# Kernel tuning notes

Measured on AMD Instinct MI355X. Metric: run time of the kernel, lower is better.

Reference implementation:

```python
import jax, jax.numpy as jnp
import numpy as np

B, H, W, C = 8, 64, 64, 512
C8, C2 = C // 8, C // 2  # f/g channels = 64, h channels = 256 (divisor = 2)


def _maxpool2x2(t):
    # [B, H, W, F] -> [B, H//2, W//2, F], valid 2x2 max pooling
    b, h, w, f = t.shape
    return t.reshape(b, h // 2, 2, w // 2, 2, f).max(axis=(2, 4))


def setup_inputs() -> dict:
    key = jax.random.key(0)
    kx, kf, kg, kh, ko, kgam = jax.random.split(key, 6)
    sf = lambda fan_in: (1.0 / np.sqrt(fan_in)).astype(np.float32)
    return {
        "x": jax.random.normal(kx, (B, H, W, C), dtype=jnp.float32),
        "wf": jax.random.normal(kf, (C, C8), dtype=jnp.float32) * sf(C),
        "wg": jax.random.normal(kg, (C, C8), dtype=jnp.float32) * sf(C),
        "wh": jax.random.normal(kh, (C, C2), dtype=jnp.float32) * sf(C),
        "wo": jax.random.normal(ko, (C2, C), dtype=jnp.float32) * sf(C2),
        "gamma": jax.random.normal(kgam, (1,), dtype=jnp.float32) * 0.1,
    }


def reference(x, wf, wg, wh, wo, gamma):
    b = x.shape[0]
    # 1x1 convs == channel matmuls
    f = _maxpool2x2(jnp.einsum("bhwc,cd->bhwd", x, wf)).reshape(b, -1, C8)  # [B, N/4, C/8]
    g = jnp.einsum("bhwc,cd->bhwd", x, wg).reshape(b, -1, C8)               # [B, N,   C/8]
    s = jnp.einsum("bqd,bkd->bqk", g, f)                                     # unscaled scores
    beta = jax.nn.softmax(s, axis=-1)
    h = _maxpool2x2(jnp.einsum("bhwc,cd->bhwd", x, wh)).reshape(b, -1, C2)  # [B, N/4, C/2]
    o = jnp.einsum("bqk,bkd->bqd", beta, h).reshape(b, H, W, C2)
    o = jnp.einsum("bhwd,dc->bhwc", o, wo)                                   # o_conv back to C
    return gamma * o + x
```

## Files before the change

kernel.cpp:

```cpp
#include <hip/hip_runtime.h>
#include <hip/hip_bf16.h>

#define NTOK 4096
#define NPOOL 1024

using short8 = __attribute__((ext_vector_type(8))) short;
using f32x4  = __attribute__((ext_vector_type(4))) float;

__device__ __forceinline__ unsigned short f2bf(float f) {
  __hip_bfloat16 h = __float2bfloat16(f);
  return __builtin_bit_cast(unsigned short, h);
}

__device__ __forceinline__ int pool_row(int bx, int m) {
  int pg = bx * 16 + (m >> 2);
  int corner = m & 3;
  int batch = pg >> 10;
  int pl = pg & 1023;
  int pi = pl >> 5, pj = pl & 31;
  return (batch << 12) + ((2 * pi + (corner >> 1)) << 6) + 2 * pj + (corner & 1);
}

__global__ __launch_bounds__(256) void pack_w(const float* __restrict__ wf,
                                              const float* __restrict__ wg,
                                              const float* __restrict__ wh,
                                              const float* __restrict__ wo,
                                              unsigned short* __restrict__ wcatT,
                                              unsigned short* __restrict__ woT) {
  int i = blockIdx.x * 256 + threadIdx.x;
  if (i < 384 * 512) {
    int n = i >> 9, k = i & 511;
    float v = (n < 64) ? wf[k * 64 + n]
            : (n < 128) ? wg[k * 64 + (n - 64)]
                        : wh[k * 256 + (n - 128)];
    wcatT[i] = f2bf(v);
  } else if (i < 384 * 512 + 512 * 256) {
    int j = i - 384 * 512;
    int n = j >> 8, k = j & 255;
    woT[j] = f2bf(wo[(size_t)k * 512 + n]);
  }
}

__global__ __launch_bounds__(512) void fgh_proj(const float* __restrict__ x,
                                                const unsigned short* __restrict__ wcatT,
                                                unsigned short* __restrict__ fB,
                                                unsigned short* __restrict__ gB,
                                                unsigned short* __restrict__ hT) {
  __shared__ unsigned short lds[33280];
  const int tid = threadIdx.x;
  const int bx = blockIdx.x;
  const int wave = tid >> 6, lane = tid & 63;
  const int col = lane & 15, rgrp = lane >> 4;
  const int wcol = wave * 48;

  {
    const int xm = tid >> 3, xk4 = (tid & 7) << 2;
    const float* xrow = x + (size_t)pool_row(bx, xm) * 512 + xk4;
    unsigned short* dst = &lds[xm * 520 + xk4];
#pragma unroll
    for (int kt = 0; kt < 16; ++kt) {
      float4 v = *(const float4*)(xrow + kt * 32);
      ushort4 o4;
      o4.x = f2bf(v.x); o4.y = f2bf(v.y); o4.z = f2bf(v.z); o4.w = f2bf(v.w);
      *(ushort4*)(dst + kt * 32) = o4;
    }
  }
  __syncthreads();

  f32x4 acc[4][3];
#pragma unroll
  for (int mt = 0; mt < 4; ++mt)
#pragma unroll
    for (int nt = 0; nt < 3; ++nt) acc[mt][nt] = (f32x4){0.f, 0.f, 0.f, 0.f};

  for (int kt = 0; kt < 16; ++kt) {
    short8 am[4];
#pragma unroll
    for (int mt = 0; mt < 4; ++mt)
      am[mt] = *(const short8*)&lds[(mt * 16 + col) * 520 + kt * 32 + rgrp * 8];
#pragma unroll
    for (int nt = 0; nt < 3; ++nt) {
      short8 bn = *(const short8*)(wcatT + (size_t)(wcol + nt * 16 + col) * 512 + kt * 32 + rgrp * 8);
#pragma unroll
      for (int mt = 0; mt < 4; ++mt)
        acc[mt][nt] = __builtin_amdgcn_mfma_f32_16x16x32_bf16(am[mt], bn, acc[mt][nt], 0, 0, 0);
    }
  }
  __syncthreads();

  unsigned short* gO = lds;
  unsigned short* fO = lds + 4608;
  unsigned short* hO = lds + 5760;
#pragma unroll
  for (int mt = 0; mt < 4; ++mt) {
#pragma unroll
    for (int nt = 0; nt < 3; ++nt) {
      int n = wcol + nt * 16 + col;
      f32x4 a = acc[mt][nt];
      if (n < 64) {
        float mx = fmaxf(fmaxf(a[0], a[1]), fmaxf(a[2], a[3]));
        fO[(mt * 4 + rgrp) * 72 + n] = f2bf(mx);
      } else if (n < 128) {
#pragma unroll
        for (int reg = 0; reg < 4; ++reg)
          gO[(mt * 16 + rgrp * 4 + reg) * 72 + (n - 64)] = f2bf(a[reg]);
      } else {
        float mx = fmaxf(fmaxf(a[0], a[1]), fmaxf(a[2], a[3]));
        hO[(n - 128) * 24 + (mt * 4 + rgrp)] = f2bf(mx);
      }
    }
  }
  __syncthreads();

  const int b = bx >> 6, pkb = (bx & 63) * 16;
  {
    int m = tid >> 3, d8 = (tid & 7) << 3;
    *(uint4*)(gB + (size_t)pool_row(bx, m) * 64 + d8) = *(const uint4*)&gO[m * 72 + d8];
  }
  if (tid < 128) {
    int pr = tid >> 3, d8 = (tid & 7) << 3;
    *(uint4*)(fB + (size_t)(bx * 16 + pr) * 64 + d8) = *(const uint4*)&fO[pr * 72 + d8];
  }
  {
    int dv = tid >> 1, p8 = (tid & 1) << 3;
    *(uint4*)(hT + (((size_t)b * 256 + dv) << 10) + pkb + p8) = *(const uint4*)&hO[dv * 24 + p8];
  }
}

__global__ __launch_bounds__(512) void attn_mfma(const __hip_bfloat16* __restrict__ G,
                                                 const __hip_bfloat16* __restrict__ F,
                                                 const __hip_bfloat16* __restrict__ HT,
                                                 const unsigned short* __restrict__ woT,
                                                 const float* __restrict__ Xres,
                                                 const float* __restrict__ gamma,
                                                 float* __restrict__ Out) {
  __shared__ unsigned short lds[33792];

  const int tid = threadIdx.x;
  const int wave = tid >> 6, lane = tid & 63;
  const int col = lane & 15;
  const int rgrp = lane >> 4;
  const int b = blockIdx.x >> 5, qt = blockIdx.x & 31;

  const unsigned short* Gb = (const unsigned short*)G + ((size_t)b * NTOK + qt * 128) * 64;
  const unsigned short* Fb = (const unsigned short*)F + (size_t)b * NPOOL * 64;
  const unsigned short* Hb = (const unsigned short*)HT + (size_t)b * 256 * NPOOL;

  short8 ag[2];
#pragma unroll
  for (int ks = 0; ks < 2; ++ks)
    ag[ks] = *(const short8*)(Gb + (size_t)(wave * 16 + col) * 64 + ks * 32 + rgrp * 8);

  f32x4 oacc[16];
#pragma unroll
  for (int t = 0; t < 16; ++t) oacc[t] = (f32x4){0.f, 0.f, 0.f, 0.f};
  float m_run[4], l_run[4];
#pragma unroll
  for (int r = 0; r < 4; ++r) { m_run[r] = -1e30f; l_run[r] = 0.f; }

  const int fk = tid >> 3, fd8 = (tid & 7) << 3;

  for (int kc = 0; kc < 16; ++kc) {
    __syncthreads();
    *(uint4*)&lds[fk * 72 + fd8] =
        *(const uint4*)(Fb + (size_t)(kc * 64 + fk) * 64 + fd8);
#pragma unroll
    for (int r = 0; r < 4; ++r) {
      int j = tid + r * 512;
      int dv = j >> 3, k8 = (j & 7) << 3;
      *(uint4*)&lds[4608 + dv * 72 + k8] =
          *(const uint4*)(Hb + (size_t)dv * NPOOL + kc * 64 + k8);
    }
    __syncthreads();

    f32x4 s[4];
#pragma unroll
    for (int t = 0; t < 4; ++t) s[t] = (f32x4){0.f, 0.f, 0.f, 0.f};
#pragma unroll
    for (int ks = 0; ks < 2; ++ks) {
#pragma unroll
      for (int t = 0; t < 4; ++t) {
        short8 bf = *(const short8*)&lds[(t * 16 + col) * 72 + ks * 32 + rgrp * 8];
        s[t] = __builtin_amdgcn_mfma_f32_16x16x32_bf16(ag[ks], bf, s[t], 0, 0, 0);
      }
    }

    float cm[4];
#pragma unroll
    for (int r = 0; r < 4; ++r) {
      cm[r] = fmaxf(fmaxf(s[0][r], s[1][r]), fmaxf(s[2][r], s[3][r]));
#pragma unroll
      for (int msk = 1; msk < 16; msk <<= 1) cm[r] = fmaxf(cm[r], __shfl_xor(cm[r], msk));
    }
    bool upd = false;
#pragma unroll
    for (int r = 0; r < 4; ++r) upd |= (cm[r] > m_run[r]);
    if (__any(upd)) {
      float alpha[4];
#pragma unroll
      for (int r = 0; r < 4; ++r) {
        float mn = fmaxf(m_run[r], cm[r]);
        alpha[r] = __expf(m_run[r] - mn);
        m_run[r] = mn;
        l_run[r] *= alpha[r];
      }
#pragma unroll
      for (int t = 0; t < 16; ++t) {
#pragma unroll
        for (int r = 0; r < 4; ++r) oacc[t][r] *= alpha[r];
      }
    }

    float rs[4] = {0.f, 0.f, 0.f, 0.f};
    const int prow = wave * 16 + rgrp * 4;
#pragma unroll
    for (int t = 0; t < 4; ++t) {
#pragma unroll
      for (int r = 0; r < 4; ++r) {
        float p = __expf(s[t][r] - m_run[r]);
        rs[r] += p;
        lds[23040 + (prow + r) * 72 + t * 16 + col] = f2bf(p);
      }
    }
#pragma unroll
    for (int r = 0; r < 4; ++r) {
#pragma unroll
      for (int msk = 1; msk < 16; msk <<= 1) rs[r] += __shfl_xor(rs[r], msk);
      l_run[r] += rs[r];
    }

    short8 ap[2];
#pragma unroll
    for (int ks = 0; ks < 2; ++ks)
      ap[ks] = *(const short8*)&lds[23040 + (wave * 16 + col) * 72 + ks * 32 + rgrp * 8];
#pragma unroll
    for (int t = 0; t < 16; ++t) {
#pragma unroll
      for (int ks = 0; ks < 2; ++ks) {
        short8 bh = *(const short8*)&lds[4608 + (t * 16 + col) * 72 + ks * 32 + rgrp * 8];
        oacc[t] = __builtin_amdgcn_mfma_f32_16x16x32_bf16(ap[ks], bh, oacc[t], 0, 0, 0);
      }
    }
  }

  float inv[4];
#pragma unroll
  for (int r = 0; r < 4; ++r) inv[r] = 1.0f / l_run[r];
  __syncthreads();
  const int qrow = wave * 16 + rgrp * 4;
#pragma unroll
  for (int t = 0; t < 16; ++t) {
#pragma unroll
    for (int r = 0; r < 4; ++r)
      lds[(qrow + r) * 264 + t * 16 + col] = f2bf(oacc[t][r] * inv[r]);
  }
  __syncthreads();

  const float gm = gamma[0];
  const int wr = (wave >> 2) * 64;
  const int wc = (wave & 3) * 64;
  const size_t rowbase = (size_t)b * NTOK + (size_t)qt * 128 + wr;
#pragma unroll
  for (int c = 0; c < 2; ++c) {
    f32x4 acc2[4][4];
#pragma unroll
    for (int mt = 0; mt < 4; ++mt)
#pragma unroll
      for (int nt = 0; nt < 4; ++nt) acc2[mt][nt] = (f32x4){0.f, 0.f, 0.f, 0.f};
#pragma unroll
    for (int kt = 0; kt < 8; ++kt) {
      short8 am[4];
#pragma unroll
      for (int mt = 0; mt < 4; ++mt)
        am[mt] = *(const short8*)&lds[(wr + mt * 16 + col) * 264 + kt * 32 + rgrp * 8];
#pragma unroll
      for (int nt = 0; nt < 4; ++nt) {
        short8 bn = *(const short8*)(woT + (size_t)(c * 256 + wc + nt * 16 + col) * 256 + kt * 32 + rgrp * 8);
#pragma unroll
        for (int mt = 0; mt < 4; ++mt)
          acc2[mt][nt] = __builtin_amdgcn_mfma_f32_16x16x32_bf16(am[mt], bn, acc2[mt][nt], 0, 0, 0);
      }
    }
#pragma unroll
    for (int mt = 0; mt < 4; ++mt) {
#pragma unroll
      for (int nt = 0; nt < 4; ++nt) {
        int n = c * 256 + wc + nt * 16 + col;
#pragma unroll
        for (int reg = 0; reg < 4; ++reg) {
          size_t off = (rowbase + mt * 16 + rgrp * 4 + reg) * 512 + n;
          Out[off] = gm * acc2[mt][nt][reg] + Xres[off];
        }
      }
    }
  }
}

extern "C" void kernel_launch(void* const* d_in, const int* in_sizes, int n_in,
                              void* d_out, int out_size, void* d_ws, size_t ws_size,
                              hipStream_t stream) {
  (void)in_sizes; (void)n_in; (void)out_size; (void)ws_size;
  const float* x     = (const float*)d_in[0];
  const float* wf    = (const float*)d_in[1];
  const float* wg    = (const float*)d_in[2];
  const float* wh    = (const float*)d_in[3];
  const float* wo    = (const float*)d_in[4];
  const float* gamma = (const float*)d_in[5];
  float* out = (float*)d_out;

  unsigned short* ws = (unsigned short*)d_ws;
  unsigned short* gB    = ws + 8388608;
  unsigned short* fB    = ws + 10485760;
  unsigned short* hT    = ws + 11010048;
  unsigned short* wcatT = ws + 13107200;
  unsigned short* woT   = ws + 13303808;

  pack_w<<<1280, dim3(256), 0, stream>>>(wf, wg, wh, wo, wcatT, woT);
  fgh_proj<<<512, dim3(512), 0, stream>>>(x, wcatT, fB, gB, hT);
  attn_mfma<<<256, dim3(512), 0, stream>>>((const __hip_bfloat16*)gB, (const __hip_bfloat16*)fB,
                                           (const __hip_bfloat16*)hT, woT, x, gamma, out);
}
```

Before: 233.8 us.

## Fuse weight pack, projection and attention into one cooperative kernel

Merges the three launches (weight packing, f/g/h projection, attention plus output conv) into a single cooperative kernel of 256 blocks separated by grid-wide syncs. Each block now handles two projection tiles, and the first tile's x load overlaps the weight packing before the first grid sync. This removes two kernel launch gaps. In exchange it adds two grid barriers, and the projection phase runs on half as many blocks with serialized tiles.

```diff
diff --git a/kernel.cpp b/kernel.cpp
--- a/kernel.cpp
+++ b/kernel.cpp
@@ -1,5 +1,8 @@
 #include <hip/hip_runtime.h>
 #include <hip/hip_bf16.h>
+#include <hip/hip_cooperative_groups.h>
+
+namespace cg = cooperative_groups;
 
 #define NTOK 4096
 #define NPOOL 1024
@@ -21,39 +24,41 @@
   return (batch << 12) + ((2 * pi + (corner >> 1)) << 6) + 2 * pj + (corner & 1);
 }
 
-__global__ __launch_bounds__(256) void pack_w(const float* __restrict__ wf,
-                                              const float* __restrict__ wg,
-                                              const float* __restrict__ wh,
-                                              const float* __restrict__ wo,
-                                              unsigned short* __restrict__ wcatT,
-                                              unsigned short* __restrict__ woT) {
-  int i = blockIdx.x * 256 + threadIdx.x;
-  if (i < 384 * 512) {
-    int n = i >> 9, k = i & 511;
-    float v = (n < 64) ? wf[k * 64 + n]
-            : (n < 128) ? wg[k * 64 + (n - 64)]
-                        : wh[k * 256 + (n - 128)];
-    wcatT[i] = f2bf(v);
-  } else if (i < 384 * 512 + 512 * 256) {
-    int j = i - 384 * 512;
-    int n = j >> 8, k = j & 255;
-    woT[j] = f2bf(wo[(size_t)k * 512 + n]);
-  }
-}
-
-__global__ __launch_bounds__(512) void fgh_proj(const float* __restrict__ x,
-                                                const unsigned short* __restrict__ wcatT,
-                                                unsigned short* __restrict__ fB,
-                                                unsigned short* __restrict__ gB,
-                                                unsigned short* __restrict__ hT) {
-  __shared__ unsigned short lds[33280];
+__global__ __launch_bounds__(512) void fused_all(
+    const float* __restrict__ x,
+    const float* __restrict__ wf,
+    const float* __restrict__ wg,
+    const float* __restrict__ wh,
+    const float* __restrict__ wo,
+    const float* __restrict__ gamma,
+    float* __restrict__ Out,
+    unsigned short* __restrict__ gB,
+    unsigned short* __restrict__ fB,
+    unsigned short* __restrict__ hT,
+    unsigned short* __restrict__ wcatT,
+    unsigned short* __restrict__ woT) {
+  __shared__ unsigned short lds[33792];
+
   const int tid = threadIdx.x;
-  const int bx = blockIdx.x;
   const int wave = tid >> 6, lane = tid & 63;
   const int col = lane & 15, rgrp = lane >> 4;
-  const int wcol = wave * 48;
+
+  for (int i = blockIdx.x * 512 + tid; i < 384 * 512 + 512 * 256; i += 256 * 512) {
+    if (i < 384 * 512) {
+      int n = i >> 9, k = i & 511;
+      float v = (n < 64) ? wf[k * 64 + n]
+              : (n < 128) ? wg[k * 64 + (n - 64)]
+                          : wh[k * 256 + (n - 128)];
+      wcatT[i] = f2bf(v);
+    } else {
+      int j = i - 384 * 512;
+      int n = j >> 8, k = j & 255;
+      woT[j] = f2bf(wo[(size_t)k * 512 + n]);
+    }
+  }
 
   {
+    const int bx = blockIdx.x * 2;
     const int xm = tid >> 3, xk4 = (tid & 7) << 2;
     const float* xrow = x + (size_t)pool_row(bx, xm) * 512 + xk4;
     unsigned short* dst = &lds[xm * 520 + xk4];
@@ -65,231 +70,242 @@
       *(ushort4*)(dst + kt * 32) = o4;
     }
   }
-  __syncthreads();
-
-  f32x4 acc[4][3];
-#pragma unroll
-  for (int mt = 0; mt < 4; ++mt)
-#pragma unroll
-    for (int nt = 0; nt < 3; ++nt) acc[mt][nt] = (f32x4){0.f, 0.f, 0.f, 0.f};
-
-  for (int kt = 0; kt < 16; ++kt) {
-    short8 am[4];
+
+  __threadfence();
+  cg::this_grid().sync();
+
+  for (int t = 0; t < 2; ++t) {
+    const int bx = blockIdx.x * 2 + t;
+    if (t == 1) {
+      __syncthreads();
+      const int xm = tid >> 3, xk4 = (tid & 7) << 2;
+      const float* xrow = x + (size_t)pool_row(bx, xm) * 512 + xk4;
+      unsigned short* dst = &lds[xm * 520 + xk4];
+#pragma unroll
+      for (int kt = 0; kt < 16; ++kt) {
+        float4 v = *(const float4*)(xrow + kt * 32);
+        ushort4 o4;
+        o4.x = f2bf(v.x); o4.y = f2bf(v.y); o4.z = f2bf(v.z); o4.w = f2bf(v.w);
+        *(ushort4*)(dst + kt * 32) = o4;
+      }
+      __syncthreads();
+    }
+    const int wcol = wave * 48;
+
+    f32x4 acc[4][3];
 #pragma unroll
     for (int mt = 0; mt < 4; ++mt)
-      am[mt] = *(const short8*)&lds[(mt * 16 + col) * 520 + kt * 32 + rgrp * 8];
-#pragma unroll
-    for (int nt = 0; nt < 3; ++nt) {
-      short8 bn = *(const short8*)(wcatT + (size_t)(wcol + nt * 16 + col) * 512 + kt * 32 + rgrp * 8);
+#pragma unroll
+      for (int nt = 0; nt < 3; ++nt) acc[mt][nt] = (f32x4){0.f, 0.f, 0.f, 0.f};
+
+    for (int kt = 0; kt < 16; ++kt) {
+      short8 am[4];
 #pragma unroll
       for (int mt = 0; mt < 4; ++mt)
-        acc[mt][nt] = __builtin_amdgcn_mfma_f32_16x16x32_bf16(am[mt], bn, acc[mt][nt], 0, 0, 0);
+        am[mt] = *(const short8*)&lds[(mt * 16 + col) * 520 + kt * 32 + rgrp * 8];
+#pragma unroll
+      for (int nt = 0; nt < 3; ++nt) {
+        short8 bn = *(const short8*)(wcatT + (size_t)(wcol + nt * 16 + col) * 512 + kt * 32 + rgrp * 8);
+#pragma unroll
+        for (int mt = 0; mt < 4; ++mt)
+          acc[mt][nt] = __builtin_amdgcn_mfma_f32_16x16x32_bf16(am[mt], bn, acc[mt][nt], 0, 0, 0);
+      }
+    }
+    __syncthreads();
+
+    unsigned short* gO = lds;
+    unsigned short* fO = lds + 4608;
+    unsigned short* hO = lds + 5760;
+#pragma unroll
+    for (int mt = 0; mt < 4; ++mt) {
+#pragma unroll
+      for (int nt = 0; nt < 3; ++nt) {
+        int n = wcol + nt * 16 + col;
+        f32x4 a = acc[mt][nt];
+        if (n < 64) {
+          float mx = fmaxf(fmaxf(a[0], a[1]), fmaxf(a[2], a[3]));
+          fO[(mt * 4 + rgrp) * 72 + n] = f2bf(mx);
+        } else if (n < 128) {
+#pragma unroll
+          for (int reg = 0; reg < 4; ++reg)
+            gO[(mt * 16 + rgrp * 4 + reg) * 72 + (n - 64)] = f2bf(a[reg]);
+        } else {
+          float mx = fmaxf(fmaxf(a[0], a[1]), fmaxf(a[2], a[3]));
+          hO[(n - 128) * 24 + (mt * 4 + rgrp)] = f2bf(mx);
+        }
+      }
+    }
+    __syncthreads();
+
+    const int b = bx >> 6, pkb = (bx & 63) * 16;
+    {
+      int m = tid >> 3, d8 = (tid & 7) << 3;
+      *(uint4*)(gB + (size_t)pool_row(bx, m) * 64 + d8) = *(const uint4*)&gO[m * 72 + d8];
+    }
+    if (tid < 128) {
+      int pr = tid >> 3, d8 = (tid & 7) << 3;
+      *(uint4*)(fB + (size_t)(bx * 16 + pr) * 64 + d8) = *(const uint4*)&fO[pr * 72 + d8];
+    }
+    {
+      int dv = tid >> 1, p8 = (tid & 1) << 3;
+      *(uint4*)(hT + (((size_t)b * 256 + dv) << 10) + pkb + p8) = *(const uint4*)&hO[dv * 24 + p8];
     }
   }
-  __syncthreads();
-
-  unsigned short* gO = lds;
-  unsigned short* fO = lds + 4608;
-  unsigned short* hO = lds + 5760;
-#pragma unroll
-  for (int mt = 0; mt < 4; ++mt) {
-#pragma unroll
-    for (int nt = 0; nt < 3; ++nt) {
-      int n = wcol + nt * 16 + col;
-      f32x4 a = acc[mt][nt];
-      if (n < 64) {
-        float mx = fmaxf(fmaxf(a[0], a[1]), fmaxf(a[2], a[3]));
-        fO[(mt * 4 + rgrp) * 72 + n] = f2bf(mx);
-      } else if (n < 128) {
-#pragma unroll
-        for (int reg = 0; reg < 4; ++reg)
-          gO[(mt * 16 + rgrp * 4 + reg) * 72 + (n - 64)] = f2bf(a[reg]);
-      } else {
-        float mx = fmaxf(fmaxf(a[0], a[1]), fmaxf(a[2], a[3]));
-        hO[(n - 128) * 24 + (mt * 4 + rgrp)] = f2bf(mx);
-      }
-    }
-  }
-  __syncthreads();
-
-  const int b = bx >> 6, pkb = (bx & 63) * 16;
+
+  __threadfence();
+  cg::this_grid().sync();
+
   {
-    int m = tid >> 3, d8 = (tid & 7) << 3;
-    *(uint4*)(gB + (size_t)pool_row(bx, m) * 64 + d8) = *(const uint4*)&gO[m * 72 + d8];
-  }
-  if (tid < 128) {
-    int pr = tid >> 3, d8 = (tid & 7) << 3;
-    *(uint4*)(fB + (size_t)(bx * 16 + pr) * 64 + d8) = *(const uint4*)&fO[pr * 72 + d8];
-  }
-  {
-    int dv = tid >> 1, p8 = (tid & 1) << 3;
-    *(uint4*)(hT + (((size_t)b * 256 + dv) << 10) + pkb + p8) = *(const uint4*)&hO[dv * 24 + p8];
-  }
-}
-
-__global__ __launch_bounds__(512) void attn_mfma(const __hip_bfloat16* __restrict__ G,
-                                                 const __hip_bfloat16* __restrict__ F,
-                                                 const __hip_bfloat16* __restrict__ HT,
-                                                 const unsigned short* __restrict__ woT,
-                                                 const float* __restrict__ Xres,
-                                                 const float* __restrict__ gamma,
-                                                 float* __restrict__ Out) {
-  __shared__ unsigned short lds[33792];
-
-  const int tid = threadIdx.x;
-  const int wave = tid >> 6, lane = tid & 63;
-  const int col = lane & 15;
-  const int rgrp = lane >> 4;
-  const int b = blockIdx.x >> 5, qt = blockIdx.x & 31;
-
-  const unsigned short* Gb = (const unsigned short*)G + ((size_t)b * NTOK + qt * 128) * 64;
-  const unsigned short* Fb = (const unsigned short*)F + (size_t)b * NPOOL * 64;
-  const unsigned short* Hb = (const unsigned short*)HT + (size_t)b * 256 * NPOOL;
-
-  short8 ag[2];
-#pragma unroll
-  for (int ks = 0; ks < 2; ++ks)
-    ag[ks] = *(const short8*)(Gb + (size_t)(wave * 16 + col) * 64 + ks * 32 + rgrp * 8);
-
-  f32x4 oacc[16];
-#pragma unroll
-  for (int t = 0; t < 16; ++t) oacc[t] = (f32x4){0.f, 0.f, 0.f, 0.f};
-  float m_run[4], l_run[4];
-#pragma unroll
-  for (int r = 0; r < 4; ++r) { m_run[r] = -1e30f; l_run[r] = 0.f; }
-
-  const int fk = tid >> 3, fd8 = (tid & 7) << 3;
-
-  for (int kc = 0; kc < 16; ++kc) {
+    const int b = blockIdx.x >> 5, qt = blockIdx.x & 31;
+    const unsigned short* Gb = gB + ((size_t)b * NTOK + qt * 128) * 64;
+    const unsigned short* Fb = fB + (size_t)b * NPOOL * 64;
+    const unsigned short* Hb = hT + (size_t)b * 256 * NPOOL;
+
+    short8 ag[2];
+#pragma unroll
+    for (int ks = 0; ks < 2; ++ks)
+      ag[ks] = *(const short8*)(Gb + (size_t)(wave * 16 + col) * 64 + ks * 32 + rgrp * 8);
+
+    f32x4 oacc[16];
+#pragma unroll
+    for (int t = 0; t < 16; ++t) oacc[t] = (f32x4){0.f, 0.f, 0.f, 0.f};
+    float m_run[4], l_run[4];
+#pragma unroll
+    for (int r = 0; r < 4; ++r) { m_run[r] = -1e30f; l_run[r] = 0.f; }
+
+    const int fk = tid >> 3, fd8 = (tid & 7) << 3;
+
+    for (int kc = 0; kc < 16; ++kc) {
+      __syncthreads();
+      *(uint4*)&lds[fk * 72 + fd8] =
+          *(const uint4*)(Fb + (size_t)(kc * 64 + fk) * 64 + fd8);
+#pragma unroll
+      for (int r = 0; r < 4; ++r) {
+        int j = tid + r * 512;
+        int dv = j >> 3, k8 = (j & 7) << 3;
+        *(uint4*)&lds[4608 + dv * 72 + k8] =
+            *(const uint4*)(Hb + (size_t)dv * NPOOL + kc * 64 + k8);
+      }
+      __syncthreads();
+
+      f32x4 s[4];
+#pragma unroll
+      for (int t = 0; t < 4; ++t) s[t] = (f32x4){0.f, 0.f, 0.f, 0.f};
+#pragma unroll
+      for (int ks = 0; ks < 2; ++ks) {
+#pragma unroll
+        for (int t = 0; t < 4; ++t) {
+          short8 bf = *(const short8*)&lds[(t * 16 + col) * 72 + ks * 32 + rgrp * 8];
+          s[t] = __builtin_amdgcn_mfma_f32_16x16x32_bf16(ag[ks], bf, s[t], 0, 0, 0);
+        }
+      }
+
+      float cm[4];
+#pragma unroll
+      for (int r = 0; r < 4; ++r) {
+        cm[r] = fmaxf(fmaxf(s[0][r], s[1][r]), fmaxf(s[2][r], s[3][r]));
+#pragma unroll
+        for (int msk = 1; msk < 16; msk <<= 1) cm[r] = fmaxf(cm[r], __shfl_xor(cm[r], msk));
+      }
+      bool upd = false;
+#pragma unroll
+      for (int r = 0; r < 4; ++r) upd |= (cm[r] > m_run[r]);
+      if (__any(upd)) {
+        float alpha[4];
+#pragma unroll
+        for (int r = 0; r < 4; ++r) {
+          float mn = fmaxf(m_run[r], cm[r]);
+          alpha[r] = __expf(m_run[r] - mn);
+          m_run[r] = mn;
+          l_run[r] *= alpha[r];
+        }
+#pragma unroll
+        for (int t = 0; t < 16; ++t) {
+#pragma unroll
+          for (int r = 0; r < 4; ++r) oacc[t][r] *= alpha[r];
+        }
+      }
+
+      float rs[4] = {0.f, 0.f, 0.f, 0.f};
+      const int prow = wave * 16 + rgrp * 4;
+#pragma unroll
+      for (int t = 0; t < 4; ++t) {
+#pragma unroll
+        for (int r = 0; r < 4; ++r) {
+          float p = __expf(s[t][r] - m_run[r]);
+          rs[r] += p;
+          lds[23040 + (prow + r) * 72 + t * 16 + col] = f2bf(p);
+        }
+      }
+#pragma unroll
+      for (int r = 0; r < 4; ++r) {
+#pragma unroll
+        for (int msk = 1; msk < 16; msk <<= 1) rs[r] += __shfl_xor(rs[r], msk);
+        l_run[r] += rs[r];
+      }
+
+      short8 ap[2];
+#pragma unroll
+      for (int ks = 0; ks < 2; ++ks)
+        ap[ks] = *(const short8*)&lds[23040 + (wave * 16 + col) * 72 + ks * 32 + rgrp * 8];
+#pragma unroll
+      for (int t = 0; t < 16; ++t) {
+#pragma unroll
+        for (int ks = 0; ks < 2; ++ks) {
+          short8 bh = *(const short8*)&lds[4608 + (t * 16 + col) * 72 + ks * 32 + rgrp * 8];
+          oacc[t] = __builtin_amdgcn_mfma_f32_16x16x32_bf16(ap[ks], bh, oacc[t], 0, 0, 0);
+        }
+      }
+    }
+
+    float inv[4];
+#pragma unroll
+    for (int r = 0; r < 4; ++r) inv[r] = 1.0f / l_run[r];
     __syncthreads();
-    *(uint4*)&lds[fk * 72 + fd8] =
-        *(const uint4*)(Fb + (size_t)(kc * 64 + fk) * 64 + fd8);
-#pragma unroll
-    for (int r = 0; r < 4; ++r) {
-      int j = tid + r * 512;
-      int dv = j >> 3, k8 = (j & 7) << 3;
-      *(uint4*)&lds[4608 + dv * 72 + k8] =
-          *(const uint4*)(Hb + (size_t)dv * NPOOL + kc * 64 + k8);
+    const int qrow = wave * 16 + rgrp * 4;
+#pragma unroll
+    for (int t = 0; t < 16; ++t) {
+#pragma unroll
+      for (int r = 0; r < 4; ++r)
+        lds[(qrow + r) * 264 + t * 16 + col] = f2bf(oacc[t][r] * inv[r]);
     }
     __syncthreads();
 
-    f32x4 s[4];
-#pragma unroll
-    for (int t = 0; t < 4; ++t) s[t] = (f32x4){0.f, 0.f, 0.f, 0.f};
-#pragma unroll
-    for (int ks = 0; ks < 2; ++ks) {
-#pragma unroll
-      for (int t = 0; t < 4; ++t) {
-        short8 bf = *(const short8*)&lds[(t * 16 + col) * 72 + ks * 32 + rgrp * 8];
-        s[t] = __builtin_amdgcn_mfma_f32_16x16x32_bf16(ag[ks], bf, s[t], 0, 0, 0);
-      }
-    }
-
-    float cm[4];
-#pragma unroll
-    for (int r = 0; r < 4; ++r) {
-      cm[r] = fmaxf(fmaxf(s[0][r], s[1][r]), fmaxf(s[2][r], s[3][r]));
-#pragma unroll
-      for (int msk = 1; msk < 16; msk <<= 1) cm[r] = fmaxf(cm[r], __shfl_xor(cm[r], msk));
-    }
-    bool upd = false;
-#pragma unroll
-    for (int r = 0; r < 4; ++r) upd |= (cm[r] > m_run[r]);
-    if (__any(upd)) {
-      float alpha[4];
-#pragma unroll
-      for (int r = 0; r < 4; ++r) {
-        float mn = fmaxf(m_run[r], cm[r]);
-        alpha[r] = __expf(m_run[r] - mn);
-        m_run[r] = mn;
-        l_run[r] *= alpha[r];
-      }
-#pragma unroll
-      for (int t = 0; t < 16; ++t) {
-#pragma unroll
-        for (int r = 0; r < 4; ++r) oacc[t][r] *= alpha[r];
-      }
-    }
-
-    float rs[4] = {0.f, 0.f, 0.f, 0.f};
-    const int prow = wave * 16 + rgrp * 4;
-#pragma unroll
-    for (int t = 0; t < 4; ++t) {
-#pragma unroll
-      for (int r = 0; r < 4; ++r) {
-        float p = __expf(s[t][r] - m_run[r]);
-        rs[r] += p;
-        lds[23040 + (prow + r) * 72 + t * 16 + col] = f2bf(p);
-      }
-    }
-#pragma unroll
-    for (int r = 0; r < 4; ++r) {
-#pragma unroll
-      for (int msk = 1; msk < 16; msk <<= 1) rs[r] += __shfl_xor(rs[r], msk);
-      l_run[r] += rs[r];
-    }
-
-    short8 ap[2];
-#pragma unroll
-    for (int ks = 0; ks < 2; ++ks)
-      ap[ks] = *(const short8*)&lds[23040 + (wave * 16 + col) * 72 + ks * 32 + rgrp * 8];
-#pragma unroll
-    for (int t = 0; t < 16; ++t) {
-#pragma unroll
-      for (int ks = 0; ks < 2; ++ks) {
-        short8 bh = *(const short8*)&lds[4608 + (t * 16 + col) * 72 + ks * 32 + rgrp * 8];
-        oacc[t] = __builtin_amdgcn_mfma_f32_16x16x32_bf16(ap[ks], bh, oacc[t], 0, 0, 0);
-      }
-    }
-  }
-
-  float inv[4];
-#pragma unroll
-  for (int r = 0; r < 4; ++r) inv[r] = 1.0f / l_run[r];
-  __syncthreads();
-  const int qrow = wave * 16 + rgrp * 4;
-#pragma unroll
-  for (int t = 0; t < 16; ++t) {
-#pragma unroll
-    for (int r = 0; r < 4; ++r)
-      lds[(qrow + r) * 264 + t * 16 + col] = f2bf(oacc[t][r] * inv[r]);
-  }
-  __syncthreads();
-
-  const float gm = gamma[0];
-  const int wr = (wave >> 2) * 64;
-  const int wc = (wave & 3) * 64;
-  const size_t rowbase = (size_t)b * NTOK + (size_t)qt * 128 + wr;
-#pragma unroll
-  for (int c = 0; c < 2; ++c) {
-    f32x4 acc2[4][4];
-#pragma unroll
-    for (int mt = 0; mt < 4; ++mt)
-#pragma unroll
-      for (int nt = 0; nt < 4; ++nt) acc2[mt][nt] = (f32x4){0.f, 0.f, 0.f, 0.f};
-#pragma unroll
-    for (int kt = 0; kt < 8; ++kt) {
-      short8 am[4];
+    const float gm = gamma[0];
+    const int wr = (wave >> 2) * 64;
+    const int wc = (wave & 3) * 64;
+    const size_t rowbase = (size_t)b * NTOK + (size_t)qt * 128 + wr;
+#pragma unroll
+    for (int c = 0; c < 2; ++c) {
+      f32x4 acc2[4][4];
 #pragma unroll
       for (int mt = 0; mt < 4; ++mt)
-        am[mt] = *(const short8*)&lds[(wr + mt * 16 + col) * 264 + kt * 32 + rgrp * 8];
-#pragma unroll
-      for (int nt = 0; nt < 4; ++nt) {
-        short8 bn = *(const short8*)(woT + (size_t)(c * 256 + wc + nt * 16 + col) * 256 + kt * 32 + rgrp * 8);
+#pragma unroll
+        for (int nt = 0; nt < 4; ++nt) acc2[mt][nt] = (f32x4){0.f, 0.f, 0.f, 0.f};
+#pragma unroll
+      for (int kt = 0; kt < 8; ++kt) {
+        short8 am[4];
 #pragma unroll
         for (int mt = 0; mt < 4; ++mt)
-          acc2[mt][nt] = __builtin_amdgcn_mfma_f32_16x16x32_bf16(am[mt], bn, acc2[mt][nt], 0, 0, 0);
-      }
-    }
-#pragma unroll
-    for (int mt = 0; mt < 4; ++mt) {
-#pragma unroll
-      for (int nt = 0; nt < 4; ++nt) {
-        int n = c * 256 + wc + nt * 16 + col;
-#pragma unroll
-        for (int reg = 0; reg < 4; ++reg) {
-          size_t off = (rowbase + mt * 16 + rgrp * 4 + reg) * 512 + n;
-          Out[off] = gm * acc2[mt][nt][reg] + Xres[off];
+          am[mt] = *(const short8*)&lds[(wr + mt * 16 + col) * 264 + kt * 32 + rgrp * 8];
+#pragma unroll
+        for (int nt = 0; nt < 4; ++nt) {
+          short8 bn = *(const short8*)(woT + (size_t)(c * 256 + wc + nt * 16 + col) * 256 + kt * 32 + rgrp * 8);
+#pragma unroll
+          for (int mt = 0; mt < 4; ++mt)
+            acc2[mt][nt] = __builtin_amdgcn_mfma_f32_16x16x32_bf16(am[mt], bn, acc2[mt][nt], 0, 0, 0);
+        }
+      }
+#pragma unroll
+      for (int mt = 0; mt < 4; ++mt) {
+#pragma unroll
+        for (int nt = 0; nt < 4; ++nt) {
+          int n = c * 256 + wc + nt * 16 + col;
+#pragma unroll
+          for (int reg = 0; reg < 4; ++reg) {
+            size_t off = (rowbase + mt * 16 + rgrp * 4 + reg) * 512 + n;
+            Out[off] = gm * acc2[mt][nt][reg] + x[off];
+          }
         }
       }
     }
@@ -315,8 +331,9 @@
   unsigned short* wcatT = ws + 13107200;
   unsigned short* woT   = ws + 13303808;
 
-  pack_w<<<1280, dim3(256), 0, stream>>>(wf, wg, wh, wo, wcatT, woT);
-  fgh_proj<<<512, dim3(512), 0, stream>>>(x, wcatT, fB, gB, hT);
-  attn_mfma<<<256, dim3(512), 0, stream>>>((const __hip_bfloat16*)gB, (const __hip_bfloat16*)fB,
-                                           (const __hip_bfloat16*)hT, woT, x, gamma, out);
+  void* args[] = {(void*)&x, (void*)&wf, (void*)&wg, (void*)&wh, (void*)&wo,
+                  (void*)&gamma, (void*)&out, (void*)&gB, (void*)&fB, (void*)&hT,
+                  (void*)&wcatT, (void*)&woT};
+  hipLaunchCooperativeKernel((const void*)fused_all, dim3(256), dim3(512),
+                             args, 0, stream);
 }
```

Result: slower. 431.6 us (+84.6%).
